# Optimization experiments

Hardware: AMD Instinct MI355X
Metric: run time of the kernel (lower is better)

## Reference

```python
import jax, jax.numpy as jnp
import numpy as np

VOCAB, EMB, HID, BATCH, SEQ = 32000, 128, 512, 64, 1024


def setup_inputs() -> dict:
    key = jax.random.key(0)
    ks = jax.random.split(key, 12)
    n = lambda k, s: jax.random.normal(k, s, dtype=jnp.float32) * 0.01
    return {
        "inputs": jax.random.randint(ks[0], (BATCH, SEQ), 0, VOCAB),
        "H0": jnp.zeros((BATCH, HID), jnp.float32),
        "C0": jnp.zeros((BATCH, HID), jnp.float32),
        "emb": n(ks[1], (VOCAB, EMB)),
        "W_xi": n(ks[2], (EMB, HID)), "W_hi": n(ks[3], (HID, HID)), "b_i": jnp.zeros(HID, jnp.float32),
        "W_xf": n(ks[4], (EMB, HID)), "W_hf": n(ks[5], (HID, HID)), "b_f": jnp.zeros(HID, jnp.float32),
        "W_xo": n(ks[6], (EMB, HID)), "W_ho": n(ks[7], (HID, HID)), "b_o": jnp.zeros(HID, jnp.float32),
        "W_xc": n(ks[8], (EMB, HID)), "W_hc": n(ks[9], (HID, HID)), "b_c": jnp.zeros(HID, jnp.float32),
        "W_hq": n(ks[10], (HID, EMB)), "b_q": jnp.zeros(EMB, jnp.float32),
        "dense_w": n(ks[11], (EMB, 1)), "dense_b": jnp.zeros(1, jnp.float32),
    }


def reference(inputs, H0, C0, emb, W_xi, W_hi, b_i, W_xf, W_hf, b_f,
              W_xo, W_ho, b_o, W_xc, W_hc, b_c, W_hq, b_q, dense_w, dense_b):
    # [B,S] -> [B,S,E] -> [S,B,E]
    x = jnp.transpose(emb[inputs], (1, 0, 2))
    # Precompute input-gate contributions in one batched GEMM per gate: [S,B,H]
    xi = x @ W_xi + b_i
    xf = x @ W_xf + b_f
    xo = x @ W_xo + b_o
    xc = x @ W_xc + b_c

    def step(carry, g):
        H, C = carry
        gi, gf, go, gc = g
        I = jax.nn.sigmoid(gi + H @ W_hi)
        F = jax.nn.sigmoid(gf + H @ W_hf)
        O = jax.nn.sigmoid(go + H @ W_ho)
        Ct = jnp.tanh(gc + H @ W_hc)
        C = F * C + I * Ct
        H = O * jnp.tanh(C)
        Y = (H @ W_hq + b_q) @ dense_w + dense_b  # [B,1]
        return (H, C), Y

    (H, C), ys = jax.lax.scan(step, (H0, C0), (xi, xf, xo, xc))
    outputs = ys.reshape(-1, 1)  # cat over time, dim 0: [S*B, 1]
    return outputs, H, C
```

## Files before the change

kernel.cpp:

```cpp
#include <hip/hip_runtime.h>


typedef short bf16x8 __attribute__((ext_vector_type(8)));
typedef float f32x4  __attribute__((ext_vector_type(4)));
typedef unsigned short ushort_t;
typedef unsigned long long u64;

#define S_LEN 1024
#define NB    64
#define NH    512
#define NE    128
#define NGRP  4
#define NWPG  32
#define NWGT  128

#define OFF_WPACK 0UL
#define OFF_XBF   2621440UL
#define OFF_EXCH  19398656UL
#define OFF_V     19660800UL
#define OFF_C0S   19662848UL
#define OFF_YPART 19663360UL

__device__ __forceinline__ ushort_t f2bf(float f){
    union { float f; unsigned u; } v; v.f = f;
    unsigned u = v.u;
    unsigned r = (u + 0x7fffu + ((u >> 16) & 1u)) >> 16;
    return (ushort_t)r;
}
__device__ __forceinline__ float sigm(float x){ return 1.f / (1.f + __expf(-x)); }
__device__ __forceinline__ float tanh_(float x){ float e = __expf(2.f * x); return (e - 1.f) / (e + 1.f); }

__global__ void pack_weights(const float* __restrict__ Wxi, const float* __restrict__ Whi,
                             const float* __restrict__ Wxf, const float* __restrict__ Whf,
                             const float* __restrict__ Wxo, const float* __restrict__ Who,
                             const float* __restrict__ Wxc, const float* __restrict__ Whc,
                             ushort_t* __restrict__ wpack){
    int bid = blockIdx.x;
    int q = bid / 20, ks = bid % 20;
    int l = threadIdx.x;
    int m = l & 15, quad = l >> 4;
    int h = q * 4 + (m >> 2), g = m & 3;
    const float* Wh = (g == 0) ? Whi : (g == 1) ? Whf : (g == 2) ? Who : Whc;
    const float* Wx = (g == 0) ? Wxi : (g == 1) ? Wxf : (g == 2) ? Wxo : Wxc;
    union { ushort_t u[8]; uint4 v4; } tmp;
    #pragma unroll
    for (int j = 0; j < 8; j++){
        int k = ks * 32 + quad * 8 + j;
        float w = (k < NH) ? Wh[(size_t)k * NH + h] : Wx[(size_t)(k - NH) * NH + h];
        tmp.u[j] = f2bf(w);
    }
    *(uint4*)(wpack + ((size_t)bid * 64 + l) * 8) = tmp.v4;
}

__global__ void prep_x(const int* __restrict__ inputs, const float* __restrict__ emb,
                       ushort_t* __restrict__ xbf){
    unsigned tid = blockIdx.x * 256u + threadIdx.x;
    unsigned e = tid & 127u;
    unsigned b = (tid >> 7) & 63u;
    unsigned s = tid >> 13;
    int row = inputs[(size_t)b * S_LEN + s];
    xbf[tid] = f2bf(emb[(size_t)row * NE + e]);
}

__global__ void prep_v(const float* __restrict__ Whq, const float* __restrict__ bq,
                       const float* __restrict__ dw, const float* __restrict__ db,
                       const float* __restrict__ H0, float* __restrict__ v,
                       float* __restrict__ c0, u64* __restrict__ exch){
    int t = threadIdx.x;
    float a = 0.f;
    for (int e = 0; e < NE; e++) a += Whq[(size_t)t * NE + e] * dw[e];
    v[t] = a;
    if (t == 0){
        float c = db[0];
        for (int e = 0; e < NE; e++) c += bq[e] * dw[e];
        *c0 = c;
    }
    int p = t & 255, half = t >> 8;
    for (int b = half * 32; b < half * 32 + 32; b++){
        unsigned lo = (unsigned)f2bf(H0[(size_t)b * NH + 2 * p]) |
                      ((unsigned)f2bf(H0[(size_t)b * NH + 2 * p + 1]) << 16);
        exch[(size_t)(b >> 4) * 8192 + (size_t)(b & 15) * 256 + p] = (u64)lo;
    }
}

__global__ void reduce_y(const float* __restrict__ ypart, const float* __restrict__ c0,
                         float* __restrict__ dout){
    int t = blockIdx.x * 256 + threadIdx.x;
    int s = t >> 6, b = t & 63;
    int g = b >> 4, bl = b & 15;
    float a = *c0;
    const float* base = ypart + (((size_t)s * NGRP + g) * NWPG) * 16 + bl;
    #pragma unroll 4
    for (int w = 0; w < NWPG; w++) a += base[w * 16];
    dout[t] = a;
}

__launch_bounds__(256, 1)
__global__ void lstm_coop(const float* __restrict__ C0,
                          const float* __restrict__ b_i, const float* __restrict__ b_f,
                          const float* __restrict__ b_o, const float* __restrict__ b_c,
                          const ushort_t* __restrict__ wpack, const ushort_t* __restrict__ xbf,
                          u64* __restrict__ exch, const float* __restrict__ v,
                          float* __restrict__ ypart, float* __restrict__ dout){
    __shared__ uint4 Hs[2][16][65];
    __shared__ uint4 Xs[3][16][17];
    __shared__ float yred[2][4][16];

    const int tid  = threadIdx.x;
    const int lane = tid & 63;
    const int wv   = tid >> 6;
    const int wg   = blockIdx.x;
    const int g    = wg >> 5;
    const int wgin = wg & 31;
    const int q    = wgin * 4 + wv;
    const int quad = lane >> 4;
    const int col  = lane & 15;
    const int h    = q * 4 + quad;
    const int b    = g * 16 + col;

    bf16x8 wfrag[20];
    #pragma unroll
    for (int ks = 0; ks < 20; ks++)
        wfrag[ks] = *(const bf16x8*)(wpack + ((size_t)(q * 20 + ks) * 64 + lane) * 8);

    const float bias0 = b_i[h], bias1 = b_f[h], bias2 = b_o[h], bias3 = b_c[h];
    const float vv = v[h];
    float C = C0[(size_t)b * NH + h];

    u64* exg = exch + (size_t)g * 8192;

    const char* HsB = (const char*)Hs;
    const char* XsB = (const char*)Xs;
    unsigned* HsD = (unsigned*)Hs;

    {
        const uint4* x0 = (const uint4*)(xbf + (size_t)(g * 16) * NE);
        Xs[0][tid >> 4][tid & 15] = x0[tid];
    }
    __syncthreads();

    for (int s = 0; s < S_LEN; s++){
        int sn = (s + 1 < S_LEN) ? s + 1 : s;
        uint4 xr = ((const uint4*)(xbf + ((size_t)sn * NB + g * 16) * NE))[tid];

        const u64* ex = exg + (size_t)(s & 1) * 4096;
        const unsigned tag = (unsigned)s;
        u64 hv[16];
        #pragma unroll
        for (int j = 0; j < 16; j++)
            hv[j] = __hip_atomic_load(ex + (size_t)j * 256 + tid, __ATOMIC_RELAXED,
                                      __HIP_MEMORY_SCOPE_AGENT);

        f32x4 acc0 = (f32x4){0.f, 0.f, 0.f, 0.f};
        f32x4 acc1 = (f32x4){0.f, 0.f, 0.f, 0.f};
        #pragma unroll
        for (int kx = 0; kx < 4; kx++){
            bf16x8 bfr = *(const bf16x8*)(XsB + (s % 3) * 4352 + col * 272 + kx * 64 + quad * 16);
            if (kx & 1) acc1 = __builtin_amdgcn_mfma_f32_16x16x32_bf16(wfrag[16 + kx], bfr, acc1, 0, 0, 0);
            else        acc0 = __builtin_amdgcn_mfma_f32_16x16x32_bf16(wfrag[16 + kx], bfr, acc0, 0, 0, 0);
        }

        for (;;){
            unsigned bad = 0;
            #pragma unroll
            for (int j = 0; j < 16; j++)
                bad |= ((unsigned)(hv[j] >> 32) != tag) ? 1u : 0u;
            if (!bad) break;
            __builtin_amdgcn_s_sleep(1);
            #pragma unroll
            for (int j = 0; j < 16; j++)
                hv[j] = __hip_atomic_load(ex + (size_t)j * 256 + tid, __ATOMIC_RELAXED,
                                          __HIP_MEMORY_SCOPE_AGENT);
        }
        #pragma unroll
        for (int j = 0; j < 16; j++)
            HsD[(s & 1) * 4160 + j * 260 + tid] = (unsigned)hv[j];
        Xs[(s + 1) % 3][tid >> 4][tid & 15] = xr;
        __syncthreads();

        if (tid < 16 && s > 0)
            ypart[(((size_t)(s - 1) * NGRP + g) * NWPG + wgin) * 16 + tid] =
                yred[(s - 1) & 1][0][tid] + yred[(s - 1) & 1][1][tid] +
                yred[(s - 1) & 1][2][tid] + yred[(s - 1) & 1][3][tid];

        #pragma unroll
        for (int ks = 0; ks < 16; ks++){
            bf16x8 bfr = *(const bf16x8*)(HsB + (s & 1) * 16640 + col * 1040 + ks * 64 + quad * 16);
            if (ks & 1) acc1 = __builtin_amdgcn_mfma_f32_16x16x32_bf16(wfrag[ks], bfr, acc1, 0, 0, 0);
            else        acc0 = __builtin_amdgcn_mfma_f32_16x16x32_bf16(wfrag[ks], bfr, acc0, 0, 0, 0);
        }
        f32x4 acc = acc0 + acc1;

        float I = sigm(acc[0] + bias0);
        float F = sigm(acc[1] + bias1);
        float O = sigm(acc[2] + bias2);
        float G = tanh_(acc[3] + bias3);
        float Cn = F * C + I * G;
        float Hn = O * tanh_(Cn);
        C = Cn;

        float Hn_hi = __shfl_xor(Hn, 16, 64);
        {
            unsigned lo = (unsigned)f2bf(Hn) | ((unsigned)f2bf(Hn_hi) << 16);
            if ((quad & 1) == 0 && s < S_LEN - 1){
                u64* ew = exg + (size_t)((s + 1) & 1) * 4096;
                unsigned idx = (unsigned)col * 256 + (unsigned)(q * 2) + (unsigned)(quad >> 1);
                u64 word = ((u64)(unsigned)(s + 1) << 32) | (u64)lo;
                __hip_atomic_store(ew + idx, word, __ATOMIC_RELAXED,
                                   __HIP_MEMORY_SCOPE_AGENT);
            }
        }

        float p = Hn * vv;
        p += __shfl_xor(p, 16, 64);
        p += __shfl_xor(p, 32, 64);
        if (quad == 0) yred[s & 1][wv][col] = p;

        if (s == S_LEN - 1){
            dout[65536 + (size_t)b * NH + h] = Hn;
            dout[98304 + (size_t)b * NH + h] = Cn;
        }
    }
    __syncthreads();
    if (tid < 16)
        ypart[(((size_t)(S_LEN - 1) * NGRP + g) * NWPG + wgin) * 16 + tid] =
            yred[(S_LEN - 1) & 1][0][tid] + yred[(S_LEN - 1) & 1][1][tid] +
            yred[(S_LEN - 1) & 1][2][tid] + yred[(S_LEN - 1) & 1][3][tid];
}

extern "C" void kernel_launch(void* const* d_in, const int* in_sizes, int n_in,
                              void* d_out, int out_size, void* d_ws, size_t ws_size,
                              hipStream_t stream){
    const int*   inputs = (const int*)  d_in[0];
    const float* H0     = (const float*)d_in[1];
    const float* C0     = (const float*)d_in[2];
    const float* emb    = (const float*)d_in[3];
    const float* W_xi   = (const float*)d_in[4];
    const float* W_hi   = (const float*)d_in[5];
    const float* b_i    = (const float*)d_in[6];
    const float* W_xf   = (const float*)d_in[7];
    const float* W_hf   = (const float*)d_in[8];
    const float* b_f    = (const float*)d_in[9];
    const float* W_xo   = (const float*)d_in[10];
    const float* W_ho   = (const float*)d_in[11];
    const float* b_o    = (const float*)d_in[12];
    const float* W_xc   = (const float*)d_in[13];
    const float* W_hc   = (const float*)d_in[14];
    const float* b_c    = (const float*)d_in[15];
    const float* W_hq   = (const float*)d_in[16];
    const float* b_q    = (const float*)d_in[17];
    const float* dw     = (const float*)d_in[18];
    const float* db     = (const float*)d_in[19];
    float* dout = (float*)d_out;

    char* ws = (char*)d_ws;
    ushort_t* wpack = (ushort_t*)(ws + OFF_WPACK);
    ushort_t* xbf   = (ushort_t*)(ws + OFF_XBF);
    u64*      exch  = (u64*)     (ws + OFF_EXCH);
    float*    v     = (float*)   (ws + OFF_V);
    float*    c0    = (float*)   (ws + OFF_C0S);
    float*    ypart = (float*)   (ws + OFF_YPART);

    pack_weights<<<dim3(128 * 20), dim3(64), 0, stream>>>(W_xi, W_hi, W_xf, W_hf,
                                                          W_xo, W_ho, W_xc, W_hc, wpack);
    prep_x<<<dim3((S_LEN * NB * NE) / 256), dim3(256), 0, stream>>>(inputs, emb, xbf);
    prep_v<<<dim3(1), dim3(512), 0, stream>>>(W_hq, b_q, dw, db, H0, v, c0, exch);

    void* args[] = { (void*)&C0, (void*)&b_i, (void*)&b_f, (void*)&b_o, (void*)&b_c,
                     (void*)&wpack, (void*)&xbf, (void*)&exch, (void*)&v,
                     (void*)&ypart, (void*)&dout };
    hipLaunchCooperativeKernel((void*)lstm_coop, dim3(NWGT), dim3(256), args, 0, stream);

    reduce_y<<<dim3(65536 / 256), dim3(256), 0, stream>>>(ypart, c0, dout);
}
```

Measured before the change: 3.124 ms.

## Fold four batch groups into each workgroup, cutting grid to 32 blocks

Each workgroup now processes all four 16-row batch groups in sequence instead of one, so 32 workgroups (not 128) run the cooperative recurrence. Each weight fragment is reused across four batch groups, and every group's spin-wait on the exchange buffer can overlap with compute on the other groups. The x-tile staging through shared memory is replaced by direct register prefetch of the next group's embedding fragment. In exchange each block does four times the serial work per step, with a __syncthreads per group. Far fewer CUs are used, which may lengthen the per-step critical path.

```diff
diff --git a/kernel.cpp b/kernel.cpp
--- a/kernel.cpp
+++ b/kernel.cpp
@@ -12,7 +12,7 @@
 #define NE    128
 #define NGRP  4
 #define NWPG  32
-#define NWGT  128
+#define NWGT  32
 
 #define OFF_WPACK 0UL
 #define OFF_XBF   2621440UL
@@ -102,21 +102,17 @@
                           const ushort_t* __restrict__ wpack, const ushort_t* __restrict__ xbf,
                           u64* __restrict__ exch, const float* __restrict__ v,
                           float* __restrict__ ypart, float* __restrict__ dout){
-    __shared__ uint4 Hs[2][16][65];
-    __shared__ uint4 Xs[3][16][17];
-    __shared__ float yred[2][4][16];
+    __shared__ uint4 Hs[NGRP][16][65];
+    __shared__ float yred[NGRP][2][4][16];
 
     const int tid  = threadIdx.x;
     const int lane = tid & 63;
     const int wv   = tid >> 6;
     const int wg   = blockIdx.x;
-    const int g    = wg >> 5;
-    const int wgin = wg & 31;
-    const int q    = wgin * 4 + wv;
+    const int q    = wg * 4 + wv;
     const int quad = lane >> 4;
     const int col  = lane & 15;
     const int h    = q * 4 + quad;
-    const int b    = g * 16 + col;
 
     bf16x8 wfrag[20];
     #pragma unroll
@@ -125,107 +121,120 @@
 
     const float bias0 = b_i[h], bias1 = b_f[h], bias2 = b_o[h], bias3 = b_c[h];
     const float vv = v[h];
-    float C = C0[(size_t)b * NH + h];
-
-    u64* exg = exch + (size_t)g * 8192;
-
+    float Cc[NGRP];
+    #pragma unroll
+    for (int g = 0; g < NGRP; g++)
+        Cc[g] = C0[(size_t)(g * 16 + col) * NH + h];
+
+    unsigned* HsD = (unsigned*)Hs;
     const char* HsB = (const char*)Hs;
-    const char* XsB = (const char*)Xs;
-    unsigned* HsD = (unsigned*)Hs;
-
+
+    bf16x8 xc0, xc1, xc2, xc3;
     {
-        const uint4* x0 = (const uint4*)(xbf + (size_t)(g * 16) * NE);
-        Xs[0][tid >> 4][tid & 15] = x0[tid];
-    }
-    __syncthreads();
+        const ushort_t* xb = xbf + (size_t)col * NE + quad * 8;
+        xc0 = *(const bf16x8*)(xb);
+        xc1 = *(const bf16x8*)(xb + 32);
+        xc2 = *(const bf16x8*)(xb + 64);
+        xc3 = *(const bf16x8*)(xb + 96);
+    }
 
     for (int s = 0; s < S_LEN; s++){
-        int sn = (s + 1 < S_LEN) ? s + 1 : s;
-        uint4 xr = ((const uint4*)(xbf + ((size_t)sn * NB + g * 16) * NE))[tid];
-
-        const u64* ex = exg + (size_t)(s & 1) * 4096;
         const unsigned tag = (unsigned)s;
-        u64 hv[16];
         #pragma unroll
-        for (int j = 0; j < 16; j++)
-            hv[j] = __hip_atomic_load(ex + (size_t)j * 256 + tid, __ATOMIC_RELAXED,
-                                      __HIP_MEMORY_SCOPE_AGENT);
-
-        f32x4 acc0 = (f32x4){0.f, 0.f, 0.f, 0.f};
-        f32x4 acc1 = (f32x4){0.f, 0.f, 0.f, 0.f};
-        #pragma unroll
-        for (int kx = 0; kx < 4; kx++){
-            bf16x8 bfr = *(const bf16x8*)(XsB + (s % 3) * 4352 + col * 272 + kx * 64 + quad * 16);
-            if (kx & 1) acc1 = __builtin_amdgcn_mfma_f32_16x16x32_bf16(wfrag[16 + kx], bfr, acc1, 0, 0, 0);
-            else        acc0 = __builtin_amdgcn_mfma_f32_16x16x32_bf16(wfrag[16 + kx], bfr, acc0, 0, 0, 0);
-        }
-
-        for (;;){
-            unsigned bad = 0;
-            #pragma unroll
-            for (int j = 0; j < 16; j++)
-                bad |= ((unsigned)(hv[j] >> 32) != tag) ? 1u : 0u;
-            if (!bad) break;
-            __builtin_amdgcn_s_sleep(1);
+        for (int g = 0; g < NGRP; g++){
+            const u64* ex = exch + (size_t)g * 8192 + (size_t)(s & 1) * 4096;
+            u64 hv[16];
             #pragma unroll
             for (int j = 0; j < 16; j++)
                 hv[j] = __hip_atomic_load(ex + (size_t)j * 256 + tid, __ATOMIC_RELAXED,
                                           __HIP_MEMORY_SCOPE_AGENT);
+
+            const int gn = (g + 1) & 3;
+            const int sn = (g == 3) ? ((s + 1 < S_LEN) ? s + 1 : s) : s;
+            const ushort_t* xb = xbf + ((size_t)sn * NB + gn * 16 + col) * NE + quad * 8;
+            bf16x8 xn0 = *(const bf16x8*)(xb);
+            bf16x8 xn1 = *(const bf16x8*)(xb + 32);
+            bf16x8 xn2 = *(const bf16x8*)(xb + 64);
+            bf16x8 xn3 = *(const bf16x8*)(xb + 96);
+
+            f32x4 acc0 = (f32x4){0.f, 0.f, 0.f, 0.f};
+            f32x4 acc1 = (f32x4){0.f, 0.f, 0.f, 0.f};
+            acc0 = __builtin_amdgcn_mfma_f32_16x16x32_bf16(wfrag[16], xc0, acc0, 0, 0, 0);
+            acc1 = __builtin_amdgcn_mfma_f32_16x16x32_bf16(wfrag[17], xc1, acc1, 0, 0, 0);
+            acc0 = __builtin_amdgcn_mfma_f32_16x16x32_bf16(wfrag[18], xc2, acc0, 0, 0, 0);
+            acc1 = __builtin_amdgcn_mfma_f32_16x16x32_bf16(wfrag[19], xc3, acc1, 0, 0, 0);
+
+            for (;;){
+                unsigned bad = 0;
+                #pragma unroll
+                for (int j = 0; j < 16; j++)
+                    bad |= ((unsigned)(hv[j] >> 32) != tag) ? 1u : 0u;
+                if (!bad) break;
+                __builtin_amdgcn_s_sleep(1);
+                #pragma unroll
+                for (int j = 0; j < 16; j++)
+                    hv[j] = __hip_atomic_load(ex + (size_t)j * 256 + tid, __ATOMIC_RELAXED,
+                                              __HIP_MEMORY_SCOPE_AGENT);
+            }
+            #pragma unroll
+            for (int j = 0; j < 16; j++)
+                HsD[g * 4160 + j * 260 + tid] = (unsigned)hv[j];
+            __syncthreads();
+
+            if (tid < 16 && s > 0)
+                ypart[(((size_t)(s - 1) * NGRP + g) * NWPG + wg) * 16 + tid] =
+                    yred[g][(s - 1) & 1][0][tid] + yred[g][(s - 1) & 1][1][tid] +
+                    yred[g][(s - 1) & 1][2][tid] + yred[g][(s - 1) & 1][3][tid];
+
+            #pragma unroll
+            for (int ks = 0; ks < 16; ks++){
+                bf16x8 bfr = *(const bf16x8*)(HsB + g * 16640 + col * 1040 + ks * 64 + quad * 16);
+                if (ks & 1) acc1 = __builtin_amdgcn_mfma_f32_16x16x32_bf16(wfrag[ks], bfr, acc1, 0, 0, 0);
+                else        acc0 = __builtin_amdgcn_mfma_f32_16x16x32_bf16(wfrag[ks], bfr, acc0, 0, 0, 0);
+            }
+            f32x4 acc = acc0 + acc1;
+
+            float I = sigm(acc[0] + bias0);
+            float F = sigm(acc[1] + bias1);
+            float O = sigm(acc[2] + bias2);
+            float G = tanh_(acc[3] + bias3);
+            float Cn = F * Cc[g] + I * G;
+            float Hn = O * tanh_(Cn);
+            Cc[g] = Cn;
+
+            float Hn_hi = __shfl_xor(Hn, 16, 64);
+            {
+                unsigned lo = (unsigned)f2bf(Hn) | ((unsigned)f2bf(Hn_hi) << 16);
+                if ((quad & 1) == 0 && s < S_LEN - 1){
+                    u64* ew = exch + (size_t)g * 8192 + (size_t)((s + 1) & 1) * 4096;
+                    unsigned idx = (unsigned)col * 256 + (unsigned)(q * 2) + (unsigned)(quad >> 1);
+                    u64 word = ((u64)(unsigned)(s + 1) << 32) | (u64)lo;
+                    __hip_atomic_store(ew + idx, word, __ATOMIC_RELAXED,
+                                       __HIP_MEMORY_SCOPE_AGENT);
+                }
+            }
+
+            float p = Hn * vv;
+            p += __shfl_xor(p, 16, 64);
+            p += __shfl_xor(p, 32, 64);
+            if (quad == 0) yred[g][s & 1][wv][col] = p;
+
+            if (s == S_LEN - 1){
+                int b = g * 16 + col;
+                dout[65536 + (size_t)b * NH + h] = Hn;
+                dout[98304 + (size_t)b * NH + h] = Cn;
+            }
+
+            xc0 = xn0; xc1 = xn1; xc2 = xn2; xc3 = xn3;
         }
-        #pragma unroll
-        for (int j = 0; j < 16; j++)
-            HsD[(s & 1) * 4160 + j * 260 + tid] = (unsigned)hv[j];
-        Xs[(s + 1) % 3][tid >> 4][tid & 15] = xr;
-        __syncthreads();
-
-        if (tid < 16 && s > 0)
-            ypart[(((size_t)(s - 1) * NGRP + g) * NWPG + wgin) * 16 + tid] =
-                yred[(s - 1) & 1][0][tid] + yred[(s - 1) & 1][1][tid] +
-                yred[(s - 1) & 1][2][tid] + yred[(s - 1) & 1][3][tid];
-
-        #pragma unroll
-        for (int ks = 0; ks < 16; ks++){
-            bf16x8 bfr = *(const bf16x8*)(HsB + (s & 1) * 16640 + col * 1040 + ks * 64 + quad * 16);
-            if (ks & 1) acc1 = __builtin_amdgcn_mfma_f32_16x16x32_bf16(wfrag[ks], bfr, acc1, 0, 0, 0);
-            else        acc0 = __builtin_amdgcn_mfma_f32_16x16x32_bf16(wfrag[ks], bfr, acc0, 0, 0, 0);
-        }
-        f32x4 acc = acc0 + acc1;
-
-        float I = sigm(acc[0] + bias0);
-        float F = sigm(acc[1] + bias1);
-        float O = sigm(acc[2] + bias2);
-        float G = tanh_(acc[3] + bias3);
-        float Cn = F * C + I * G;
-        float Hn = O * tanh_(Cn);
-        C = Cn;
-
-        float Hn_hi = __shfl_xor(Hn, 16, 64);
-        {
-            unsigned lo = (unsigned)f2bf(Hn) | ((unsigned)f2bf(Hn_hi) << 16);
-            if ((quad & 1) == 0 && s < S_LEN - 1){
-                u64* ew = exg + (size_t)((s + 1) & 1) * 4096;
-                unsigned idx = (unsigned)col * 256 + (unsigned)(q * 2) + (unsigned)(quad >> 1);
-                u64 word = ((u64)(unsigned)(s + 1) << 32) | (u64)lo;
-                __hip_atomic_store(ew + idx, word, __ATOMIC_RELAXED,
-                                   __HIP_MEMORY_SCOPE_AGENT);
-            }
-        }
-
-        float p = Hn * vv;
-        p += __shfl_xor(p, 16, 64);
-        p += __shfl_xor(p, 32, 64);
-        if (quad == 0) yred[s & 1][wv][col] = p;
-
-        if (s == S_LEN - 1){
-            dout[65536 + (size_t)b * NH + h] = Hn;
-            dout[98304 + (size_t)b * NH + h] = Cn;
-        }
     }
     __syncthreads();
-    if (tid < 16)
-        ypart[(((size_t)(S_LEN - 1) * NGRP + g) * NWPG + wgin) * 16 + tid] =
-            yred[(S_LEN - 1) & 1][0][tid] + yred[(S_LEN - 1) & 1][1][tid] +
-            yred[(S_LEN - 1) & 1][2][tid] + yred[(S_LEN - 1) & 1][3][tid];
+    if (tid < 64){
+        int gg = tid >> 4, t = tid & 15;
+        ypart[(((size_t)(S_LEN - 1) * NGRP + gg) * NWPG + wg) * 16 + t] =
+            yred[gg][(S_LEN - 1) & 1][0][t] + yred[gg][(S_LEN - 1) & 1][1][t] +
+            yred[gg][(S_LEN - 1) & 1][2][t] + yred[gg][(S_LEN - 1) & 1][3][t];
+    }
 }
 
 extern "C" void kernel_launch(void* const* d_in, const int* in_sizes, int n_in,
```

New measurement: 8.775 ms. 2.81x slower.

## Consolidate LSTM recurrence into 32 workgroups of 1024 threads

Applied to the files above, without the earlier changes.

Each LSTM workgroup now holds 16 waves instead of 4, so the grid shrinks from 128 to 32 workgroups. Each workgroup loads the exchanged hidden state once for four times as many hidden units, cutting redundant global polling traffic and the number of agents in the per-step cross-workgroup exchange. The partial-y reduction is widened to match. The cost is fewer CUs in use, and with launch bounds of 1024 each wave's 20-fragment weight set must still fit in its register budget, which could cause spilling.

```diff
diff --git a/kernel.cpp b/kernel.cpp
--- a/kernel.cpp
+++ b/kernel.cpp
@@ -11,8 +11,8 @@
 #define NH    512
 #define NE    128
 #define NGRP  4
-#define NWPG  32
-#define NWGT  128
+#define NWPG  8
+#define NWGT  32
 
 #define OFF_WPACK 0UL
 #define OFF_XBF   2621440UL
@@ -90,12 +90,12 @@
     int g = b >> 4, bl = b & 15;
     float a = *c0;
     const float* base = ypart + (((size_t)s * NGRP + g) * NWPG) * 16 + bl;
-    #pragma unroll 4
+    #pragma unroll
     for (int w = 0; w < NWPG; w++) a += base[w * 16];
     dout[t] = a;
 }
 
-__launch_bounds__(256, 1)
+__launch_bounds__(1024, 1)
 __global__ void lstm_coop(const float* __restrict__ C0,
                           const float* __restrict__ b_i, const float* __restrict__ b_f,
                           const float* __restrict__ b_o, const float* __restrict__ b_c,
@@ -104,15 +104,15 @@
                           float* __restrict__ ypart, float* __restrict__ dout){
     __shared__ uint4 Hs[2][16][65];
     __shared__ uint4 Xs[3][16][17];
-    __shared__ float yred[2][4][16];
+    __shared__ float yred[2][16][16];
 
     const int tid  = threadIdx.x;
     const int lane = tid & 63;
     const int wv   = tid >> 6;
     const int wg   = blockIdx.x;
-    const int g    = wg >> 5;
-    const int wgin = wg & 31;
-    const int q    = wgin * 4 + wv;
+    const int g    = wg >> 3;
+    const int wgin = wg & 7;
+    const int q    = wgin * 16 + wv;
     const int quad = lane >> 4;
     const int col  = lane & 15;
     const int h    = q * 4 + quad;
@@ -133,22 +133,25 @@
     const char* XsB = (const char*)Xs;
     unsigned* HsD = (unsigned*)Hs;
 
-    {
+    if (tid < 256){
         const uint4* x0 = (const uint4*)(xbf + (size_t)(g * 16) * NE);
         Xs[0][tid >> 4][tid & 15] = x0[tid];
     }
     __syncthreads();
 
     for (int s = 0; s < S_LEN; s++){
-        int sn = (s + 1 < S_LEN) ? s + 1 : s;
-        uint4 xr = ((const uint4*)(xbf + ((size_t)sn * NB + g * 16) * NE))[tid];
+        uint4 xr = {0, 0, 0, 0};
+        if (tid < 256){
+            int sn = (s + 1 < S_LEN) ? s + 1 : s;
+            xr = ((const uint4*)(xbf + ((size_t)sn * NB + g * 16) * NE))[tid];
+        }
 
         const u64* ex = exg + (size_t)(s & 1) * 4096;
         const unsigned tag = (unsigned)s;
-        u64 hv[16];
-        #pragma unroll
-        for (int j = 0; j < 16; j++)
-            hv[j] = __hip_atomic_load(ex + (size_t)j * 256 + tid, __ATOMIC_RELAXED,
+        u64 hv[4];
+        #pragma unroll
+        for (int j = 0; j < 4; j++)
+            hv[j] = __hip_atomic_load(ex + (size_t)j * 1024 + tid, __ATOMIC_RELAXED,
                                       __HIP_MEMORY_SCOPE_AGENT);
 
         f32x4 acc0 = (f32x4){0.f, 0.f, 0.f, 0.f};
@@ -163,25 +166,27 @@
         for (;;){
             unsigned bad = 0;
             #pragma unroll
-            for (int j = 0; j < 16; j++)
+            for (int j = 0; j < 4; j++)
                 bad |= ((unsigned)(hv[j] >> 32) != tag) ? 1u : 0u;
             if (!bad) break;
             __builtin_amdgcn_s_sleep(1);
             #pragma unroll
-            for (int j = 0; j < 16; j++)
-                hv[j] = __hip_atomic_load(ex + (size_t)j * 256 + tid, __ATOMIC_RELAXED,
+            for (int j = 0; j < 4; j++)
+                hv[j] = __hip_atomic_load(ex + (size_t)j * 1024 + tid, __ATOMIC_RELAXED,
                                           __HIP_MEMORY_SCOPE_AGENT);
         }
         #pragma unroll
-        for (int j = 0; j < 16; j++)
-            HsD[(s & 1) * 4160 + j * 260 + tid] = (unsigned)hv[j];
-        Xs[(s + 1) % 3][tid >> 4][tid & 15] = xr;
+        for (int j = 0; j < 4; j++)
+            HsD[(s & 1) * 4160 + (j * 4 + (tid >> 8)) * 260 + (tid & 255)] = (unsigned)hv[j];
+        if (tid < 256) Xs[(s + 1) % 3][tid >> 4][tid & 15] = xr;
         __syncthreads();
 
-        if (tid < 16 && s > 0)
-            ypart[(((size_t)(s - 1) * NGRP + g) * NWPG + wgin) * 16 + tid] =
-                yred[(s - 1) & 1][0][tid] + yred[(s - 1) & 1][1][tid] +
-                yred[(s - 1) & 1][2][tid] + yred[(s - 1) & 1][3][tid];
+        if (tid < 16 && s > 0){
+            float yy = 0.f;
+            #pragma unroll
+            for (int w = 0; w < 16; w++) yy += yred[(s - 1) & 1][w][tid];
+            ypart[(((size_t)(s - 1) * NGRP + g) * NWPG + wgin) * 16 + tid] = yy;
+        }
 
         #pragma unroll
         for (int ks = 0; ks < 16; ks++){
@@ -222,10 +227,12 @@
         }
     }
     __syncthreads();
-    if (tid < 16)
-        ypart[(((size_t)(S_LEN - 1) * NGRP + g) * NWPG + wgin) * 16 + tid] =
-            yred[(S_LEN - 1) & 1][0][tid] + yred[(S_LEN - 1) & 1][1][tid] +
-            yred[(S_LEN - 1) & 1][2][tid] + yred[(S_LEN - 1) & 1][3][tid];
+    if (tid < 16){
+        float yy = 0.f;
+        #pragma unroll
+        for (int w = 0; w < 16; w++) yy += yred[(S_LEN - 1) & 1][w][tid];
+        ypart[(((size_t)(S_LEN - 1) * NGRP + g) * NWPG + wgin) * 16 + tid] = yy;
+    }
 }
 
 extern "C" void kernel_launch(void* const* d_in, const int* in_sizes, int n_in,
@@ -269,7 +276,7 @@
     void* args[] = { (void*)&C0, (void*)&b_i, (void*)&b_f, (void*)&b_o, (void*)&b_c,
                      (void*)&wpack, (void*)&xbf, (void*)&exch, (void*)&v,
                      (void*)&ypart, (void*)&dout };
-    hipLaunchCooperativeKernel((void*)lstm_coop, dim3(NWGT), dim3(256), args, 0, stream);
+    hipLaunchCooperativeKernel((void*)lstm_coop, dim3(NWGT), dim3(1024), args, 0, stream);
 
     reduce_y<<<dim3(65536 / 256), dim3(256), 0, stream>>>(ypart, c0, dout);
 }
```

After: 4.237 ms. 1.36x slower.
